# Optimization experiments

Hardware: AMD Instinct MI355X
Metric: run time of the kernel (lower is better)

## Reference

```python
import jax, jax.numpy as jnp
import numpy as np

DIM_T = 128
N_USER = 50000
N_ITEM = 50000
E = 600000
D_USER = 64
D_ITEM = 32
D_HID = 256
N_IN_USER = 25000
N_IN_ITEM = 25000
N_LAYERS = 2


def timestep_embedding(t, dim, max_period=10000.0):
    # improved-diffusion sinusoidal embedding: [cos | sin]
    half = dim // 2
    freqs = jnp.exp(-jnp.log(jnp.asarray(max_period, jnp.float32)) * jnp.arange(half, dtype=jnp.float32) / half)
    args = t.astype(jnp.float32)[:, None] * freqs  # [N, half]
    return jnp.concatenate([jnp.cos(args), jnp.sin(args)], axis=-1)


def sage_conv(x_src, x_dst, src, dst, W_nbr, W_root, b, n_dst):
    # PyG SAGEConv (aggr='mean'): lin_l(mean_j x_src[j]) + lin_r(x_dst)
    summed = jax.ops.segment_sum(x_src[src], dst, num_segments=n_dst)  # gather + scatter-add
    cnt = jax.ops.segment_sum(jnp.ones(src.shape, x_src.dtype), dst, num_segments=n_dst)
    mean = summed / jnp.maximum(cnt, 1.0)[:, None]
    return mean @ W_nbr + x_dst @ W_root + b


def mlp3(x, W1, b1, W2, b2, W3, b3):
    # rtdl baseline MLP: Linear->ReLU (x2) -> head Linear (dropout=0)
    h = jax.nn.relu(x @ W1 + b1)
    h = jax.nn.relu(h @ W2 + b2)
    return h @ W3 + b3


def _forward(x_user, x_item, t_user, t_item, e_ui_src, e_ui_dst, e_iu_src, e_iu_dst,
             te_W1, te_b1, te_W2, te_b2, proj_Wu, proj_bu, proj_Wi, proj_bi,
             sage_Wnbr, sage_Wroot, sage_b,
             mlp_u_W1, mlp_u_b1, mlp_u_W2, mlp_u_b2, mlp_u_W3, mlp_u_b3,
             mlp_i_W1, mlp_i_b1, mlp_i_W2, mlp_i_b2, mlp_i_W3, mlp_i_b3):
    def time_mlp(t):
        e = timestep_embedding(t, DIM_T)
        return jax.nn.silu(e @ te_W1 + te_b1) @ te_W2 + te_b2

    h_u = x_user @ proj_Wu + proj_bu + time_mlp(t_user)
    h_i = x_item @ proj_Wi + proj_bi + time_mlp(t_item)

    for l in range(N_LAYERS):  # loop over structurally distinct layers only
        new_i = sage_conv(h_u, h_i, e_ui_src, e_ui_dst, sage_Wnbr[l, 0], sage_Wroot[l, 0], sage_b[l, 0], N_ITEM)
        new_u = sage_conv(h_i, h_u, e_iu_src, e_iu_dst, sage_Wnbr[l, 1], sage_Wroot[l, 1], sage_b[l, 1], N_USER)
        h_u, h_i = jax.nn.relu(new_u), jax.nn.relu(new_i)

    out_u = mlp3(h_u[:N_IN_USER], mlp_u_W1, mlp_u_b1, mlp_u_W2, mlp_u_b2, mlp_u_W3, mlp_u_b3)
    out_i = mlp3(h_i[:N_IN_ITEM], mlp_i_W1, mlp_i_b1, mlp_i_W2, mlp_i_b2, mlp_i_W3, mlp_i_b3)
    return out_u, out_i


def setup_inputs() -> dict:
    key = jax.random.key(0)
    ks = iter(jax.random.split(key, 40))
    s = 0.02

    def W(shape):
        return jax.random.normal(next(ks), shape, jnp.float32) * s

    def zb(n):
        return jnp.zeros((n,), jnp.float32)

    inp = {}
    inp["x_user"] = jax.random.normal(next(ks), (N_USER, D_USER), jnp.float32)
    inp["x_item"] = jax.random.normal(next(ks), (N_ITEM, D_ITEM), jnp.float32)
    inp["t_user"] = jax.random.randint(next(ks), (N_USER,), 0, 1000, jnp.int32)
    inp["t_item"] = jax.random.randint(next(ks), (N_ITEM,), 0, 1000, jnp.int32)
    inp["e_ui_src"] = jax.random.randint(next(ks), (E,), 0, N_USER, jnp.int32)
    inp["e_ui_dst"] = jax.random.randint(next(ks), (E,), 0, N_ITEM, jnp.int32)
    inp["e_iu_src"] = jax.random.randint(next(ks), (E,), 0, N_ITEM, jnp.int32)
    inp["e_iu_dst"] = jax.random.randint(next(ks), (E,), 0, N_USER, jnp.int32)
    inp["te_W1"] = W((DIM_T, DIM_T)); inp["te_b1"] = zb(DIM_T)
    inp["te_W2"] = W((DIM_T, DIM_T)); inp["te_b2"] = zb(DIM_T)
    inp["proj_Wu"] = W((D_USER, DIM_T)); inp["proj_bu"] = zb(DIM_T)
    inp["proj_Wi"] = W((D_ITEM, DIM_T)); inp["proj_bi"] = zb(DIM_T)
    inp["sage_Wnbr"] = W((N_LAYERS, 2, DIM_T, DIM_T))   # [layer, edge_type(0:u->i,1:i->u), C, C]
    inp["sage_Wroot"] = W((N_LAYERS, 2, DIM_T, DIM_T))
    inp["sage_b"] = jnp.zeros((N_LAYERS, 2, DIM_T), jnp.float32)
    inp["mlp_u_W1"] = W((DIM_T, D_HID)); inp["mlp_u_b1"] = zb(D_HID)
    inp["mlp_u_W2"] = W((D_HID, D_HID)); inp["mlp_u_b2"] = zb(D_HID)
    inp["mlp_u_W3"] = W((D_HID, D_USER)); inp["mlp_u_b3"] = zb(D_USER)
    inp["mlp_i_W1"] = W((DIM_T, D_HID)); inp["mlp_i_b1"] = zb(D_HID)
    inp["mlp_i_W2"] = W((D_HID, D_HID)); inp["mlp_i_b2"] = zb(D_HID)
    inp["mlp_i_W3"] = W((D_HID, D_ITEM)); inp["mlp_i_b3"] = zb(D_ITEM)
    return inp


def reference(x_user, x_item, t_user, t_item, e_ui_src, e_ui_dst, e_iu_src, e_iu_dst,
              te_W1, te_b1, te_W2, te_b2, proj_Wu, proj_bu, proj_Wi, proj_bi,
              sage_Wnbr, sage_Wroot, sage_b,
              mlp_u_W1, mlp_u_b1, mlp_u_W2, mlp_u_b2, mlp_u_W3, mlp_u_b3,
              mlp_i_W1, mlp_i_b1, mlp_i_W2, mlp_i_b2, mlp_i_W3, mlp_i_b3):
    return _forward(x_user, x_item, t_user, t_item, e_ui_src, e_ui_dst, e_iu_src, e_iu_dst,
                    te_W1, te_b1, te_W2, te_b2, proj_Wu, proj_bu, proj_Wi, proj_bi,
                    sage_Wnbr, sage_Wroot, sage_b,
                    mlp_u_W1, mlp_u_b1, mlp_u_W2, mlp_u_b2, mlp_u_W3, mlp_u_b3,
                    mlp_i_W1, mlp_i_b1, mlp_i_W2, mlp_i_b2, mlp_i_W3, mlp_i_b3)
```

## Files before the change

### kernel.cpp

```cpp
#include <hip/hip_runtime.h>
#include <math.h>

#define NEDGE 600000
#define NUSER 50000
#define NITEM 50000
#define DIMT  128
#define NIN   25000
#define NTVAL 1000

typedef unsigned short ushort_t;
typedef __attribute__((ext_vector_type(8))) short bf16x8;
typedef __attribute__((ext_vector_type(8))) unsigned short us8;
typedef __attribute__((ext_vector_type(4))) float f32x4;
typedef __attribute__((ext_vector_type(4))) unsigned upk4;

__device__ __forceinline__ unsigned pack_hl(float f) {
    unsigned u = __float_as_uint(f);
    unsigned r = u + 0x7fffu + ((u >> 16) & 1u);
    unsigned h = (r >> 16) & 0xffffu;
    float fh = __uint_as_float(h << 16);
    float fl = f - fh;
    unsigned ul = __float_as_uint(fl);
    unsigned rl = ul + 0x7fffu + ((ul >> 16) & 1u);
    return h | (rl & 0xffff0000u);
}
__device__ __forceinline__ void split_bf16(float f, ushort_t& h, ushort_t& l) {
    unsigned p = pack_hl(f);
    h = (ushort_t)(p & 0xffffu);
    l = (ushort_t)(p >> 16);
}
__device__ __forceinline__ float upk_val(unsigned u) {
    return __uint_as_float(u << 16) + __uint_as_float(u & 0xffff0000u);
}

__device__ __forceinline__ void unpack_frag(upk4 p0, upk4 p1, bf16x8& ah, bf16x8& al) {
    upk4 h, l;
#if __has_builtin(__builtin_amdgcn_perm)
    h.x = __builtin_amdgcn_perm(p0.y, p0.x, 0x05040100u);
    h.y = __builtin_amdgcn_perm(p0.w, p0.z, 0x05040100u);
    h.z = __builtin_amdgcn_perm(p1.y, p1.x, 0x05040100u);
    h.w = __builtin_amdgcn_perm(p1.w, p1.z, 0x05040100u);
    l.x = __builtin_amdgcn_perm(p0.y, p0.x, 0x07060302u);
    l.y = __builtin_amdgcn_perm(p0.w, p0.z, 0x07060302u);
    l.z = __builtin_amdgcn_perm(p1.y, p1.x, 0x07060302u);
    l.w = __builtin_amdgcn_perm(p1.w, p1.z, 0x07060302u);
#else
    h.x = (p0.x & 0xffffu) | (p0.y << 16);
    h.y = (p0.z & 0xffffu) | (p0.w << 16);
    h.z = (p1.x & 0xffffu) | (p1.y << 16);
    h.w = (p1.z & 0xffffu) | (p1.w << 16);
    l.x = (p0.x >> 16) | (p0.y & 0xffff0000u);
    l.y = (p0.z >> 16) | (p0.w & 0xffff0000u);
    l.z = (p1.x >> 16) | (p1.y & 0xffff0000u);
    l.w = (p1.z >> 16) | (p1.w & 0xffff0000u);
#endif
    ah = __builtin_bit_cast(bf16x8, h);
    al = __builtin_bit_cast(bf16x8, l);
}

__device__ __forceinline__ size_t sm_addr(int row, int k, int nr) {
    return ((size_t)(k >> 4) * (unsigned)nr + (unsigned)row) * 16 + (k & 15);
}

struct WDesc { const float* src; int K; int N; unsigned dst; };
struct WDescs { WDesc d[16]; };

#define PREP_LUT  500
#define PREP_CVTW 256
#define PREP_CVTX 512
#define HIST_CH   64
#define PREP_HIST (8 * HIST_CH)
#define DRANGE    (NUSER / 8)

__global__ __launch_bounds__(256) void prep_kernel(
        WDescs wd, ushort_t* __restrict__ WT,
        const float* __restrict__ teW1, const float* __restrict__ teb1,
        const float* __restrict__ teW2, const float* __restrict__ teb2,
        float* __restrict__ Tlut,
        const float* __restrict__ xu, const float* __restrict__ xi,
        unsigned* __restrict__ xup, unsigned* __restrict__ xip,
        const int* __restrict__ s0, const int* __restrict__ d0,
        const int* __restrict__ s1, const int* __restrict__ d1,
        unsigned* __restrict__ pe0, unsigned* __restrict__ pe1,
        int* __restrict__ cnt2) {
    __shared__ float sE[2][128];
    __shared__ float sH[2][128];
    int b = blockIdx.x;
    int tid = threadIdx.x;
    if (b < PREP_LUT) {
        int r = tid >> 7, j = tid & 127;
        int t = b * 2 + r;
        {
            int jj = j & 63;
            const float Lf = 9.210340371976184f;
            float p  = -Lf * (float)jj;
            float ae = p * 0.015625f;
            float freq = (float)exp((double)ae);
            float arg  = (float)t * freq;
            double a = (double)arg;
            sE[r][j] = (j < 64) ? (float)cos(a) : (float)sin(a);
        }
        __syncthreads();
        {
            float acc = teb1[j];
            for (int k = 0; k < 128; ++k) acc = fmaf(sE[r][k], teW1[k * 128 + j], acc);
            float s = 1.f / (1.f + expf(-acc));
            sH[r][j] = acc * s;
        }
        __syncthreads();
        {
            float acc = teb2[j];
            for (int k = 0; k < 128; ++k) acc = fmaf(sH[r][k], teW2[k * 128 + j], acc);
            Tlut[(size_t)t * 128 + j] = acc;
        }
    } else if (b < PREP_LUT + PREP_CVTW) {
        int g = (b - PREP_LUT) * 256 + tid;
        int gs = PREP_CVTW * 256;
#pragma unroll 1
        for (int i = 0; i < 16; ++i) {
            const WDesc w = wd.d[i];
            int sz = w.K * w.N;
            int ng = sz >> 3;
            int kshift = 31 - __clz(w.K);
            int kmask = w.K - 1;
            ushort_t* ph = WT + w.dst;
            ushort_t* pl = ph + sz;
            for (int t = g; t < ng; t += gs) {
                int e8 = t << 3;
                int n  = e8 >> kshift;
                int k0 = e8 & kmask;
                us8 hb, lb;
#pragma unroll
                for (int j = 0; j < 8; ++j) {
                    ushort_t h, l;
                    split_bf16(w.src[(size_t)(k0 + j) * w.N + n], h, l);
                    hb[j] = h; lb[j] = l;
                }
                *reinterpret_cast<us8*>(ph + e8) = hb;
                *reinterpret_cast<us8*>(pl + e8) = lb;
            }
        }
    } else if (b < PREP_LUT + PREP_CVTW + PREP_CVTX) {
        int g = (b - PREP_LUT - PREP_CVTW) * 256 + tid;
        int gs = PREP_CVTX * 256;
        for (int i = g; i < NUSER * 64; i += gs) {
            int row = i >> 6, k = i & 63;
            xup[sm_addr(row, k, NUSER)] = pack_hl(xu[i]);
        }
        for (int i = g; i < NITEM * 32; i += gs) {
            int row = i >> 5, k = i & 31;
            xip[sm_addr(row, k, NITEM)] = pack_hl(xi[i]);
        }
        for (int i = g; i < NEDGE; i += gs) {
            pe0[i] = ((unsigned)d0[i] & 0xffffu) | ((unsigned)s0[i] << 16);
            pe1[i] = ((unsigned)d1[i] & 0xffffu) | ((unsigned)s1[i] << 16);
        }
    } else {
        int hb = b - PREP_LUT - PREP_CVTW - PREP_CVTX;
        int r = hb & 7, c = hb >> 3;
        int lo = r * DRANGE, hi = lo + DRANGE;
        const int epb = (NEDGE + HIST_CH - 1) / HIST_CH;
        int e0 = c * epb, e1 = min(e0 + epb, NEDGE);
        for (int e = e0 + tid; e < e1; e += 256) {
            int d = d0[e];
            if (d >= lo && d < hi) atomicAdd(&cnt2[d], 1);
        }
        for (int e = e0 + tid; e < e1; e += 256) {
            int d = d1[e];
            if (d >= lo && d < hi) atomicAdd(&cnt2[NUSER + d], 1);
        }
    }
}

#define ACT_NONE 0
#define ACT_RELU 1

struct MProb {
    const unsigned *A1p; int K1;
    const unsigned *A2p; int K2;
    const ushort_t *W1, *W2;
    const float* bias; const float* res; const int* tidx;
    float* Yf; unsigned* Yp;
    int M; int nblk; int anr; int ynr;
};

template<int NOUT, int ACT, bool DUAL, int RESMODE, int OUTMODE>
__global__ __launch_bounds__(256)
void mgemm_kernel(MProb q0, MProb q1) {
    constexpr int WN  = (NOUT >= 64) ? 64 : NOUT;
    constexpr int NWC = NOUT / WN;
    constexpr int NWR = 4 / NWC;
    constexpr int BM  = NWR * 64;
    constexpr int NF  = WN / 16;

    const bool firstp = (blockIdx.x < (unsigned)q0.nblk);
    const MProb& q = firstp ? q0 : q1;
    const int bid = firstp ? blockIdx.x : (blockIdx.x - q0.nblk);

    const int w    = threadIdx.x >> 6;
    const int lane = threadIdx.x & 63;
    const int wc   = w % NWC;
    const int wr   = w / NWC;
    const int mw   = bid * BM + wr * 64;
    const int nw   = wc * WN;
    const int lr   = lane & 15;
    const int lkg  = lane >> 4;

    f32x4 acc[4][NF];
#pragma unroll
    for (int i = 0; i < 4; ++i)
#pragma unroll
        for (int j = 0; j < NF; ++j) acc[i][j] = (f32x4)0.f;

    const int nkt1 = q.K1 / 32;
    const int nkt  = nkt1 + (DUAL ? q.K2 / 32 : 0);

    upk4 pa[4][2];
    auto loadA = [&](int kt) {
        const unsigned* Ap; int kk;
        if (!DUAL || kt < nkt1) { Ap = q.A1p; kk = kt * 32; }
        else                    { Ap = q.A2p; kk = (kt - nkt1) * 32; }
        const int kb = kk + lkg * 8;
#pragma unroll
        for (int mf = 0; mf < 4; ++mf) {
            int row = mw + mf * 16 + lr;
            if (row < q.M) {
                const upk4* p = reinterpret_cast<const upk4*>(Ap + sm_addr(row, kb, q.anr));
                pa[mf][0] = p[0]; pa[mf][1] = p[1];
            } else {
                pa[mf][0] = (upk4)0u; pa[mf][1] = (upk4)0u;
            }
        }
    };

    loadA(0);
#pragma unroll 1
    for (int kt = 0; kt < nkt; ++kt) {
        bf16x8 a_h[4], a_l[4];
#pragma unroll
        for (int mf = 0; mf < 4; ++mf) unpack_frag(pa[mf][0], pa[mf][1], a_h[mf], a_l[mf]);
        if (kt + 1 < nkt) loadA(kt + 1);

        const ushort_t* Wh; int K, kk;
        if (!DUAL || kt < nkt1) { Wh = q.W1; K = q.K1; kk = kt * 32; }
        else                    { Wh = q.W2; K = q.K2; kk = (kt - nkt1) * 32; }
        const ushort_t* Wl = Wh + (size_t)NOUT * K;
        const int kb = kk + lkg * 8;
        bf16x8 b_h[NF], b_l[NF];
#pragma unroll
        for (int nf = 0; nf < NF; ++nf) {
            int col = nw + nf * 16 + lr;
            b_h[nf] = *reinterpret_cast<const bf16x8*>(Wh + (size_t)col * K + kb);
            b_l[nf] = *reinterpret_cast<const bf16x8*>(Wl + (size_t)col * K + kb);
        }
#pragma unroll
        for (int mf = 0; mf < 4; ++mf)
#pragma unroll
            for (int nf = 0; nf < NF; ++nf) {
                acc[mf][nf] = __builtin_amdgcn_mfma_f32_16x16x32_bf16(a_h[mf], b_h[nf], acc[mf][nf], 0, 0, 0);
                acc[mf][nf] = __builtin_amdgcn_mfma_f32_16x16x32_bf16(a_h[mf], b_l[nf], acc[mf][nf], 0, 0, 0);
                acc[mf][nf] = __builtin_amdgcn_mfma_f32_16x16x32_bf16(a_l[mf], b_h[nf], acc[mf][nf], 0, 0, 0);
            }
    }

    __syncthreads();

    float bcol[NF];
#pragma unroll
    for (int nf = 0; nf < NF; ++nf) bcol[nf] = q.bias[nw + nf * 16 + lr];

#pragma unroll
    for (int mf = 0; mf < 4; ++mf) {
#pragma unroll
        for (int r = 0; r < 4; ++r) {
            int row = mw + mf * 16 + lkg * 4 + r;
            if (row >= q.M) continue;
            const float* rp = nullptr;
            if (RESMODE == 2) { int tv = q.tidx[row]; rp = q.res + (size_t)tv * NOUT; }
#pragma unroll
            for (int nf = 0; nf < NF; ++nf) {
                int col = nw + nf * 16 + lr;
                float v = acc[mf][nf][r] + bcol[nf];
                if (RESMODE == 2) v += rp[col];
                if (ACT == ACT_RELU) v = fmaxf(v, 0.f);
                if (OUTMODE & 1) q.Yf[(size_t)row * NOUT + col] = v;
                if (OUTMODE & 2) q.Yp[sm_addr(row, col, q.ynr)] = pack_hl(v);
            }
        }
    }
}

#define SCAN_CHUNK 2048
#define GSCAN 25

__global__ __launch_bounds__(256) void scan1x2_kernel(const int* __restrict__ cnt2,
                                                      int* __restrict__ bsum2) {
    __shared__ int sdata[256];
    int p = blockIdx.x / GSCAN, b = blockIdx.x % GSCAN;
    const int* cnt = cnt2 + p * NUSER;
    int base = b * SCAN_CHUNK + threadIdx.x * 8;
    int s = 0;
#pragma unroll
    for (int j = 0; j < 8; ++j) { int i = base + j; if (i < NUSER) s += cnt[i]; }
    sdata[threadIdx.x] = s;
    __syncthreads();
    for (int st = 128; st > 0; st >>= 1) {
        if ((int)threadIdx.x < st) sdata[threadIdx.x] += sdata[threadIdx.x + st];
        __syncthreads();
    }
    if (threadIdx.x == 0) bsum2[p * 32 + b] = sdata[0];
}

__global__ __launch_bounds__(256) void scan3x2_kernel(const int* __restrict__ cnt2,
                                                      const int* __restrict__ bsum2,
                                                      int* __restrict__ off_ui,
                                                      int* __restrict__ off_iu,
                                                      int* __restrict__ wp2) {
    __shared__ int sth[256];
    int p = blockIdx.x / GSCAN, b = blockIdx.x % GSCAN;
    const int* cnt = cnt2 + p * NUSER;
    int* offs = p ? off_iu : off_ui;
    int* wp = wp2 + p * NUSER;
    int t = threadIdx.x;
    int boff = 0;
    for (int i = 0; i < b; ++i) boff += bsum2[p * 32 + i];
    int base = b * SCAN_CHUNK + t * 8;
    int loc[8];
    int s = 0;
#pragma unroll
    for (int j = 0; j < 8; ++j) {
        int i = base + j;
        int v = (i < NUSER) ? cnt[i] : 0;
        loc[j] = s; s += v;
    }
    sth[t] = s;
    __syncthreads();
    for (int st = 1; st < 256; st <<= 1) {
        int v = (t >= st) ? sth[t - st] : 0;
        __syncthreads();
        sth[t] += v;
        __syncthreads();
    }
    int exc = (t == 0) ? 0 : sth[t - 1];
#pragma unroll
    for (int j = 0; j < 8; ++j) {
        int i = base + j;
        if (i < NUSER) { int o = boff + exc + loc[j]; offs[i] = o; wp[i] = o; }
    }
    if (b == GSCAN - 1 && t == 255) offs[NUSER] = boff + sth[255];
}

#define FILL_CH 256

__global__ __launch_bounds__(256) void fill2p_kernel(
        const unsigned* __restrict__ pe0, const unsigned* __restrict__ pe1,
        int* __restrict__ wp2,
        ushort_t* __restrict__ bkt0, ushort_t* __restrict__ bkt1) {
    int r = blockIdx.x & 7, c = blockIdx.x >> 3;
    int lo = r * DRANGE, hi = lo + DRANGE;
    const int epb = (NEDGE + FILL_CH - 1) / FILL_CH;
    int e0 = c * epb, e1 = min(e0 + epb, NEDGE);
#pragma unroll 4
    for (int e = e0 + (int)threadIdx.x; e < e1; e += 256) {
        unsigned p = pe0[e];
        int d = (int)(p & 0xffffu);
        if (d >= lo && d < hi) { int pos = atomicAdd(&wp2[d], 1); bkt0[pos] = (ushort_t)(p >> 16); }
    }
#pragma unroll 4
    for (int e = e0 + (int)threadIdx.x; e < e1; e += 256) {
        unsigned p = pe1[e];
        int d = (int)(p & 0xffffu);
        if (d >= lo && d < hi) { int pos = atomicAdd(&wp2[NUSER + d], 1); bkt1[pos] = (ushort_t)(p >> 16); }
    }
}

struct GProb { const unsigned* Hp; const int* offs; const ushort_t* bkt; unsigned* Op; int N; };
#define GCH64 782

__global__ __launch_bounds__(256)
void gather_slice4_kernel(GProb g0, GProb g1) {
    int s = blockIdx.x & 7;
    int chunk = blockIdx.x >> 3;
    int grp = threadIdx.x >> 2;
    int c   = threadIdx.x & 3;
    const bool firstp = (chunk < GCH64);
    const GProb& g = firstp ? g0 : g1;
    int row = (firstp ? chunk : chunk - GCH64) * 64 + grp;
    if (row >= g.N) return;
    int beg = g.offs[row], end = g.offs[row + 1];
    const upk4* __restrict__ base =
        reinterpret_cast<const upk4*>(g.Hp + ((size_t)s * NUSER) * 16) + c;
    float s0 = 0.f, s1 = 0.f, s2 = 0.f, s3 = 0.f;
    int e = beg;
    for (; e + 1 < end; e += 2) {
        int r0 = g.bkt[e], r1 = g.bkt[e + 1];
        upk4 v0 = base[(size_t)r0 * 4];
        upk4 v1 = base[(size_t)r1 * 4];
        s0 += upk_val(v0.x) + upk_val(v1.x);
        s1 += upk_val(v0.y) + upk_val(v1.y);
        s2 += upk_val(v0.z) + upk_val(v1.z);
        s3 += upk_val(v0.w) + upk_val(v1.w);
    }
    if (e < end) {
        upk4 v = base[(size_t)g.bkt[e] * 4];
        s0 += upk_val(v.x); s1 += upk_val(v.y);
        s2 += upk_val(v.z); s3 += upk_val(v.w);
    }
    float d = (float)max(end - beg, 1);
    upk4 o;
    o.x = pack_hl(s0 / d); o.y = pack_hl(s1 / d);
    o.z = pack_hl(s2 / d); o.w = pack_hl(s3 / d);
    *(reinterpret_cast<upk4*>(g.Op + ((size_t)s * NUSER + row) * 16) + c) = o;
}

extern "C" void kernel_launch(void* const* d_in, const int* in_sizes, int n_in,
                              void* d_out, int out_size, void* d_ws, size_t ws_size,
                              hipStream_t stream) {
    const float* x_user  = (const float*)d_in[0];
    const float* x_item  = (const float*)d_in[1];
    const int*   t_user  = (const int*)d_in[2];
    const int*   t_item  = (const int*)d_in[3];
    const int*   eui_src = (const int*)d_in[4];
    const int*   eui_dst = (const int*)d_in[5];
    const int*   eiu_src = (const int*)d_in[6];
    const int*   eiu_dst = (const int*)d_in[7];
    const float* te_W1 = (const float*)d_in[8];  const float* te_b1 = (const float*)d_in[9];
    const float* te_W2 = (const float*)d_in[10]; const float* te_b2 = (const float*)d_in[11];
    const float* proj_Wu = (const float*)d_in[12]; const float* proj_bu = (const float*)d_in[13];
    const float* proj_Wi = (const float*)d_in[14]; const float* proj_bi = (const float*)d_in[15];
    const float* sage_Wnbr  = (const float*)d_in[16];
    const float* sage_Wroot = (const float*)d_in[17];
    const float* sage_b     = (const float*)d_in[18];
    const float* mu_W1 = (const float*)d_in[19]; const float* mu_b1 = (const float*)d_in[20];
    const float* mu_W2 = (const float*)d_in[21]; const float* mu_b2 = (const float*)d_in[22];
    const float* mu_W3 = (const float*)d_in[23]; const float* mu_b3 = (const float*)d_in[24];
    const float* mi_W1 = (const float*)d_in[25]; const float* mi_b1 = (const float*)d_in[26];
    const float* mi_W2 = (const float*)d_in[27]; const float* mi_b2 = (const float*)d_in[28];
    const float* mi_W3 = (const float*)d_in[29]; const float* mi_b3 = (const float*)d_in[30];

    float* out_u = (float*)d_out;
    float* out_i = out_u + (size_t)NIN * 64;

    const size_t PL = (size_t)NUSER * DIMT;
    float* Tlut = (float*)d_ws;
    unsigned* up = (unsigned*)(Tlut + NTVAL * 128);
    unsigned* Hp_u = up;
    unsigned* Hp_i = up + PL;
    unsigned* G0   = up + 2 * PL;
    unsigned* Gp_i = G0;
    unsigned* Gp_u = G0 + PL;
    ushort_t* WT   = (ushort_t*)(up + 4 * PL);

    WDescs wd;
    unsigned woff[16];
    unsigned off = 0; int wi = 0;
    auto addw = [&](const float* src, int K, int N) {
        wd.d[wi].src = src; wd.d[wi].K = K; wd.d[wi].N = N; wd.d[wi].dst = off;
        woff[wi] = off; off += 2u * K * N; ++wi;
    };
    addw(proj_Wu, 64, 128);
    addw(proj_Wi, 32, 128);
    for (int l = 0; l < 2; ++l)
        for (int e = 0; e < 2; ++e)
            addw(sage_Wnbr + (size_t)(l * 2 + e) * DIMT * DIMT, 128, 128);
    for (int l = 0; l < 2; ++l)
        for (int e = 0; e < 2; ++e)
            addw(sage_Wroot + (size_t)(l * 2 + e) * DIMT * DIMT, 128, 128);
    addw(mu_W1, 128, 256);
    addw(mu_W2, 256, 256);
    addw(mu_W3, 256, 64);
    addw(mi_W1, 128, 256);
    addw(mi_W2, 256, 256);
    addw(mi_W3, 256, 32);

    int* ip = (int*)(WT + off + (off & 1));
    int* cnt2   = ip;  ip += 2 * NUSER;
    int* wp2    = ip;  ip += 2 * NUSER;
    int* off_ui = ip;  ip += NUSER + 1;
    int* off_iu = ip;  ip += NUSER + 1;
    int* bsum2  = ip;  ip += 64;
    unsigned* pe0 = (unsigned*)ip;  ip += NEDGE;
    unsigned* pe1 = (unsigned*)ip;  ip += NEDGE;
    ushort_t* bkt_ui = (ushort_t*)ip;
    ushort_t* bkt_iu = bkt_ui + NEDGE;

    MProb qn = {}; qn.nblk = 0;

    unsigned* xu_p = G0;
    unsigned* xi_p = G0 + PL;

    hipMemsetAsync(cnt2, 0, 2 * NUSER * sizeof(int), stream);
    prep_kernel<<<PREP_LUT + PREP_CVTW + PREP_CVTX + PREP_HIST, 256, 0, stream>>>(
        wd, WT, te_W1, te_b1, te_W2, te_b2, Tlut,
        x_user, x_item, xu_p, xi_p,
        eui_src, eui_dst, eiu_src, eiu_dst, pe0, pe1, cnt2);

    scan1x2_kernel<<<2 * GSCAN, 256, 0, stream>>>(cnt2, bsum2);
    scan3x2_kernel<<<2 * GSCAN, 256, 0, stream>>>(cnt2, bsum2, off_ui, off_iu, wp2);
    fill2p_kernel<<<8 * FILL_CH, 256, 0, stream>>>(pe0, pe1, wp2, bkt_ui, bkt_iu);

    {
        MProb qu = {}; MProb qi = {};
        qu.A1p = xu_p; qu.K1 = 64;
        qu.W1 = WT + woff[0]; qu.bias = proj_bu; qu.res = Tlut; qu.tidx = t_user;
        qu.Yp = Hp_u; qu.M = NUSER; qu.nblk = (NUSER + 127) / 128;
        qu.anr = NUSER; qu.ynr = NUSER;
        qi.A1p = xi_p; qi.K1 = 32;
        qi.W1 = WT + woff[1]; qi.bias = proj_bi; qi.res = Tlut; qi.tidx = t_item;
        qi.Yp = Hp_i; qi.M = NITEM; qi.nblk = (NITEM + 127) / 128;
        qi.anr = NITEM; qi.ynr = NITEM;
        mgemm_kernel<128, ACT_NONE, false, 2, 2><<<qu.nblk + qi.nblk, 256, 0, stream>>>(qu, qi);
    }

    for (int l = 0; l < 2; ++l) {
        {
            GProb gi = { Hp_u, off_ui, bkt_ui, Gp_i, NITEM };
            GProb gu = { Hp_i, off_iu, bkt_iu, Gp_u, NUSER };
            gather_slice4_kernel<<<8 * 2 * GCH64, 256, 0, stream>>>(gi, gu);
        }
        {
            MProb qi = {}; MProb qu = {};
            qi.A1p = Gp_i; qi.K1 = 128;
            qi.A2p = Hp_i; qi.K2 = 128;
            qi.W1 = WT + woff[2 + l * 2 + 0]; qi.W2 = WT + woff[6 + l * 2 + 0];
            qi.bias = sage_b + (size_t)(l * 2 + 0) * DIMT;
            qi.Yp = Hp_i; qi.M = NITEM; qi.nblk = (NITEM + 127) / 128;
            qi.anr = NUSER; qi.ynr = NUSER;
            qu.A1p = Gp_u; qu.K1 = 128;
            qu.A2p = Hp_u; qu.K2 = 128;
            qu.W1 = WT + woff[2 + l * 2 + 1]; qu.W2 = WT + woff[6 + l * 2 + 1];
            qu.bias = sage_b + (size_t)(l * 2 + 1) * DIMT;
            qu.Yp = Hp_u; qu.M = NUSER; qu.nblk = (NUSER + 127) / 128;
            qu.anr = NUSER; qu.ynr = NUSER;
            mgemm_kernel<128, ACT_RELU, true, 0, 2><<<qi.nblk + qu.nblk, 256, 0, stream>>>(qi, qu);
        }
    }

    unsigned* Tp_u = G0;
    unsigned* Tp_i = G0 + PL;
    {
        MProb qu = {}; MProb qi = {};
        qu.A1p = Hp_u; qu.K1 = 128;
        qu.W1 = WT + woff[10]; qu.bias = mu_b1;
        qu.Yp = Tp_u; qu.M = NIN; qu.nblk = (NIN + 63) / 64;
        qu.anr = NUSER; qu.ynr = NIN;
        qi.A1p = Hp_i; qi.K1 = 128;
        qi.W1 = WT + woff[13]; qi.bias = mi_b1;
        qi.Yp = Tp_i; qi.M = NIN; qi.nblk = (NIN + 63) / 64;
        qi.anr = NUSER; qi.ynr = NIN;
        mgemm_kernel<256, ACT_RELU, false, 0, 2><<<qu.nblk + qi.nblk, 256, 0, stream>>>(qu, qi);
    }
    {
        MProb qu = {}; MProb qi = {};
        qu.A1p = Tp_u; qu.K1 = 256;
        qu.W1 = WT + woff[11]; qu.bias = mu_b2;
        qu.Yp = Tp_u; qu.M = NIN; qu.nblk = (NIN + 63) / 64;
        qu.anr = NIN; qu.ynr = NIN;
        qi.A1p = Tp_i; qi.K1 = 256;
        qi.W1 = WT + woff[14]; qi.bias = mi_b2;
        qi.Yp = Tp_i; qi.M = NIN; qi.nblk = (NIN + 63) / 64;
        qi.anr = NIN; qi.ynr = NIN;
        mgemm_kernel<256, ACT_RELU, false, 0, 2><<<qu.nblk + qi.nblk, 256, 0, stream>>>(qu, qi);
    }
    {
        MProb q = {};
        q.A1p = Tp_u; q.K1 = 256;
        q.W1 = WT + woff[12]; q.bias = mu_b3;
        q.Yf = out_u; q.M = NIN; q.nblk = (NIN + 255) / 256;
        q.anr = NIN; q.ynr = NIN;
        mgemm_kernel<64, ACT_NONE, false, 0, 1><<<q.nblk, 256, 0, stream>>>(q, qn);
    }
    {
        MProb q = {};
        q.A1p = Tp_i; q.K1 = 256;
        q.W1 = WT + woff[15]; q.bias = mi_b3;
        q.Yf = out_i; q.M = NIN; q.nblk = (NIN + 255) / 256;
        q.anr = NIN; q.ynr = NIN;
        mgemm_kernel<32, ACT_NONE, false, 0, 1><<<q.nblk, 256, 0, stream>>>(q, qn);
    }

    (void)in_sizes; (void)n_in; (void)out_size; (void)ws_size;
}
```

Before: 515.9 us.

## Sort destination rows by degree to balance gather workload across lanes

Adds a degree histogram and counting-sort pass that builds a permutation of destination rows grouped by in-degree. The gather kernel then processes rows in permuted order so rows with similar edge counts share a wavefront, reducing divergence in the per-row loop. It also raises the histogram chunk count in the prep kernel. The cost is two extra small kernel launches, atomics into global bins, and scattered row access in the gather.

Result: slower. 729.7 us (+41.5%).

```diff
diff --git a/kernel.cpp b/kernel.cpp
--- a/kernel.cpp
+++ b/kernel.cpp
@@ -68,7 +68,7 @@
 #define PREP_LUT  500
 #define PREP_CVTW 256
 #define PREP_CVTX 512
-#define HIST_CH   64
+#define HIST_CH   256
 #define PREP_HIST (8 * HIST_CH)
 #define DRANGE    (NUSER / 8)
 
@@ -292,6 +292,7 @@
 
 #define SCAN_CHUNK 2048
 #define GSCAN 25
+#define DBINS 64
 
 __global__ __launch_bounds__(256) void scan1x2_kernel(const int* __restrict__ cnt2,
                                                       int* __restrict__ bsum2) {
@@ -315,13 +316,16 @@
                                                       const int* __restrict__ bsum2,
                                                       int* __restrict__ off_ui,
                                                       int* __restrict__ off_iu,
-                                                      int* __restrict__ wp2) {
+                                                      int* __restrict__ wp2,
+                                                      int* __restrict__ dh) {
     __shared__ int sth[256];
+    __shared__ int ldh[DBINS];
     int p = blockIdx.x / GSCAN, b = blockIdx.x % GSCAN;
     const int* cnt = cnt2 + p * NUSER;
     int* offs = p ? off_iu : off_ui;
     int* wp = wp2 + p * NUSER;
     int t = threadIdx.x;
+    if (t < DBINS) ldh[t] = 0;
     int boff = 0;
     for (int i = 0; i < b; ++i) boff += bsum2[p * 32 + i];
     int base = b * SCAN_CHUNK + t * 8;
@@ -345,9 +349,42 @@
 #pragma unroll
     for (int j = 0; j < 8; ++j) {
         int i = base + j;
-        if (i < NUSER) { int o = boff + exc + loc[j]; offs[i] = o; wp[i] = o; }
+        if (i < NUSER) {
+            int v = cnt[i];
+            int o = boff + exc + loc[j];
+            offs[i] = o; wp[i] = o;
+            atomicAdd(&ldh[min(v, DBINS - 1)], 1);
+        }
     }
     if (b == GSCAN - 1 && t == 255) offs[NUSER] = boff + sth[255];
+    __syncthreads();
+    if (t < DBINS && ldh[t]) atomicAdd(&dh[p * DBINS + t], ldh[t]);
+}
+
+__global__ void dsort2_kernel(const int* __restrict__ dh, int* __restrict__ dwp) {
+    int p = threadIdx.x;
+    if (p < 2) {
+        int run = 0;
+        for (int i = 0; i < DBINS; ++i) { dwp[p * DBINS + i] = run; run += dh[p * DBINS + i]; }
+    }
+}
+
+__global__ __launch_bounds__(256) void dsort3_kernel(const int* __restrict__ cnt2,
+                                                     int* __restrict__ dwp,
+                                                     int* __restrict__ perm2) {
+    int p = blockIdx.x / GSCAN, b = blockIdx.x % GSCAN;
+    const int* cnt = cnt2 + p * NUSER;
+    int* perm = perm2 + p * NUSER;
+    int base = b * SCAN_CHUNK + threadIdx.x * 8;
+#pragma unroll
+    for (int j = 0; j < 8; ++j) {
+        int i = base + j;
+        if (i < NUSER) {
+            int d = min(cnt[i], DBINS - 1);
+            int pos = atomicAdd(&dwp[p * DBINS + d], 1);
+            perm[pos] = i;
+        }
+    }
 }
 
 #define FILL_CH 256
@@ -374,7 +411,8 @@
     }
 }
 
-struct GProb { const unsigned* Hp; const int* offs; const ushort_t* bkt; unsigned* Op; int N; };
+struct GProb { const unsigned* Hp; const int* offs; const ushort_t* bkt;
+               const int* perm; unsigned* Op; int N; };
 #define GCH64 782
 
 __global__ __launch_bounds__(256)
@@ -385,8 +423,9 @@
     int c   = threadIdx.x & 3;
     const bool firstp = (chunk < GCH64);
     const GProb& g = firstp ? g0 : g1;
-    int row = (firstp ? chunk : chunk - GCH64) * 64 + grp;
-    if (row >= g.N) return;
+    int idx = (firstp ? chunk : chunk - GCH64) * 64 + grp;
+    if (idx >= g.N) return;
+    int row = g.perm[idx];
     int beg = g.offs[row], end = g.offs[row + 1];
     const upk4* __restrict__ base =
         reinterpret_cast<const upk4*>(g.Hp + ((size_t)s * NUSER) * 16) + c;
@@ -475,10 +514,13 @@
 
     int* ip = (int*)(WT + off + (off & 1));
     int* cnt2   = ip;  ip += 2 * NUSER;
+    int* dh     = ip;  ip += 2 * DBINS;
+    int* dwp    = ip;  ip += 2 * DBINS;
     int* wp2    = ip;  ip += 2 * NUSER;
     int* off_ui = ip;  ip += NUSER + 1;
     int* off_iu = ip;  ip += NUSER + 1;
     int* bsum2  = ip;  ip += 64;
+    int* perm2  = ip;  ip += 2 * NUSER;
     unsigned* pe0 = (unsigned*)ip;  ip += NEDGE;
     unsigned* pe1 = (unsigned*)ip;  ip += NEDGE;
     ushort_t* bkt_ui = (ushort_t*)ip;
@@ -489,14 +531,16 @@
     unsigned* xu_p = G0;
     unsigned* xi_p = G0 + PL;
 
-    hipMemsetAsync(cnt2, 0, 2 * NUSER * sizeof(int), stream);
+    hipMemsetAsync(cnt2, 0, (2 * NUSER + 2 * DBINS) * sizeof(int), stream);
     prep_kernel<<<PREP_LUT + PREP_CVTW + PREP_CVTX + PREP_HIST, 256, 0, stream>>>(
         wd, WT, te_W1, te_b1, te_W2, te_b2, Tlut,
         x_user, x_item, xu_p, xi_p,
         eui_src, eui_dst, eiu_src, eiu_dst, pe0, pe1, cnt2);
 
     scan1x2_kernel<<<2 * GSCAN, 256, 0, stream>>>(cnt2, bsum2);
-    scan3x2_kernel<<<2 * GSCAN, 256, 0, stream>>>(cnt2, bsum2, off_ui, off_iu, wp2);
+    scan3x2_kernel<<<2 * GSCAN, 256, 0, stream>>>(cnt2, bsum2, off_ui, off_iu, wp2, dh);
+    dsort2_kernel<<<1, 64, 0, stream>>>(dh, dwp);
+    dsort3_kernel<<<2 * GSCAN, 256, 0, stream>>>(cnt2, dwp, perm2);
     fill2p_kernel<<<8 * FILL_CH, 256, 0, stream>>>(pe0, pe1, wp2, bkt_ui, bkt_iu);
 
     {
@@ -514,8 +558,8 @@
 
     for (int l = 0; l < 2; ++l) {
         {
-            GProb gi = { Hp_u, off_ui, bkt_ui, Gp_i, NITEM };
-            GProb gu = { Hp_i, off_iu, bkt_iu, Gp_u, NUSER };
+            GProb gi = { Hp_u, off_ui, bkt_ui, perm2,         Gp_i, NITEM };
+            GProb gu = { Hp_i, off_iu, bkt_iu, perm2 + NUSER, Gp_u, NUSER };
             gather_slice4_kernel<<<8 * 2 * GCH64, 256, 0, stream>>>(gi, gu);
         }
         {
```
